# Kernel optimization log

Measured on AMD Instinct MI355X. Metric: run time of the kernel, lower is better.

The kernel has to match this reference:

```python
import jax, jax.numpy as jnp
import numpy as np

B = 2048        # batch
C = 64          # args.embed_size (channel dim; attention runs over this axis)
N = 11          # spatial rows per window
D = 11          # args.hsi_windowSize
SA = N * D      # args.size_SA = 121, Linear in/out size
HID = 128       # args.hid_router
NUM_PATH = 4    # num_out_path


def setup_inputs() -> dict:
    key = jax.random.key(0)
    ks = jax.random.split(key, 12)
    w = lambda k, shape: (jax.random.normal(k, shape, dtype=jnp.float32) * 0.05)
    return {
        "lidar": jax.random.normal(ks[0], (B, C, N, D), dtype=jnp.float32),
        "hsi": jax.random.normal(ks[1], (B, C, N, D), dtype=jnp.float32),
        # Cross_Self_attention linears (shared module, used in both directions)
        "Wq": w(ks[2], (SA, SA)), "bq": jnp.zeros((SA,), jnp.float32),
        "Wk": w(ks[3], (SA, SA)), "bk": jnp.zeros((SA,), jnp.float32),
        "Wv": w(ks[4], (SA, SA)), "bv": jnp.zeros((SA,), jnp.float32),
        # Router MLP: Linear(2C, HID) -> ReLU -> Linear(HID, NUM_PATH) -> softmax
        "Wr1": w(ks[5], (2 * C, HID)), "br1": jnp.zeros((HID,), jnp.float32),
        "Wr2": w(ks[6], (HID, NUM_PATH)), "br2": jnp.zeros((NUM_PATH,), jnp.float32),
        # 1x1 Conv2d(2C -> C): pure channel mixing
        "Wc": w(ks[7], (C, 2 * C)), "bc": jnp.zeros((C,), jnp.float32),
    }


def reference(lidar, hsi, Wq, bq, Wk, bk, Wv, bv, Wr1, br1, Wr2, br2, Wc, bc):
    def cross_sa(x, y):
        # x, y: [B, C, SA]; Linear acts on last dim (size_SA)
        q = x @ Wq.T + bq                                   # [B, C, SA]
        k = x @ Wk.T + bk                                   # [B, C, SA]
        v = y @ Wv.T + bv                                   # [B, C, SA]
        scores = jnp.einsum('bhs,bgs->bhg', q, k)           # [B, C, C] attn over channels
        probs = jax.nn.softmax(scores, axis=-1)
        # custom: attn @ (Q * V) elementwise gate instead of attn @ V
        return jnp.einsum('bhg,bgs->bhs', probs, q * v)     # [B, C, SA]
        # dropout(0.5) is identity in eval mode

    # router on channel-concat of raw inputs
    pooled = jnp.concatenate([lidar, hsi], axis=1).mean(axis=(2, 3))   # [B, 2C]
    path_prob = jax.nn.softmax(jax.nn.relu(pooled @ Wr1 + br1) @ Wr2 + br2, axis=-1)

    l = lidar.reshape(B, C, SA)
    h = hsi.reshape(B, C, SA)
    h_emb = cross_sa(l, h).reshape(B, C, N, D)
    l_emb = cross_sa(h, l).reshape(B, C, N, D)

    cat = jnp.concatenate([l_emb, h_emb], axis=1)                       # [B, 2C, N, D]
    emb = jnp.einsum('oc,bchw->bohw', Wc, cat) + bc[None, :, None, None]
    return (emb, path_prob)
```

## Files before the change

kernel.cpp:

```cpp
#include <hip/hip_runtime.h>
#include <hip/hip_bf16.h>

#define NB 2048
#define SA 121
#define EMB_TOTAL (NB * 64 * SA)

typedef short bf16x8 __attribute__((ext_vector_type(8)));
typedef float f32x4  __attribute__((ext_vector_type(4)));
typedef unsigned int u32x2 __attribute__((ext_vector_type(2)));

__device__ __forceinline__ short f2bf(float f) {
    union { __hip_bfloat16 h; short s; } u;
    u.h = __float2bfloat16(f);
    return u.s;
}
__device__ __forceinline__ float bf2f(short s) {
    union { unsigned u; float f; } v; v.u = ((unsigned)(unsigned short)s) << 16;
    return v.f;
}
__device__ __forceinline__ unsigned pack2(float a, float b) {
    union { __hip_bfloat16 h[2]; unsigned u; } p;
    p.h[0] = __float2bfloat16(a);
    p.h[1] = __float2bfloat16(b);
    return p.u;
}

#define MFMA(a, b, c) __builtin_amdgcn_mfma_f32_16x16x32_bf16((a), (b), (c), 0, 0, 0)

__global__ void convert_weights(const float* __restrict__ Wq, const float* __restrict__ Wk,
                                const float* __restrict__ Wv, const float* __restrict__ Wc,
                                short* __restrict__ ws) {
    int i = blockIdx.x * 256 + threadIdx.x;
    if (i < 49152) {
        int m = i / 16384;
        const float* W = (m == 0) ? Wq : ((m == 1) ? Wk : Wv);
        int j = i & 16383;
        int r = j >> 7, c = j & 127;
        float v = (r < SA && c < SA) ? W[r * SA + c] : 0.f;
        ws[i] = f2bf(v);
    } else {
        int j = i - 49152;
        ws[i] = f2bf(Wc[j]);
    }
}

__launch_bounds__(256, 2)
__global__ void fused_kernel(const float* __restrict__ lidar, const float* __restrict__ hsi,
                             const float* __restrict__ bq, const float* __restrict__ bk,
                             const float* __restrict__ bv,
                             const float* __restrict__ Wr1, const float* __restrict__ br1,
                             const float* __restrict__ Wr2, const float* __restrict__ br2,
                             const float* __restrict__ bc,
                             const short* __restrict__ wsb, float* __restrict__ out) {
    __shared__ __align__(16) short sA[64 * 136];
    __shared__ __align__(16) short sB[64 * 136];
    __shared__ __align__(16) short sC[64 * 136];
    __shared__ __align__(16) short sD[128 * 72];
    __shared__ __align__(16) short sE[64 * 72];
    __shared__ float sR[260];

    const int tid  = threadIdx.x;
    const int b    = blockIdx.x;
    const int lane = tid & 63;
    const int wid  = tid >> 6;
    const int l16  = lane & 15;
    const int g16  = lane >> 4;

    const short* WQ = wsb;
    const short* WK = wsb + 16384;
    const short* WV = wsb + 32768;
    const short* WC = wsb + 49152;

    bf16x8 wqf[2][4], wkf[2][4], wvf[2][4];
    #pragma unroll
    for (int nn = 0; nn < 2; ++nn) {
        const int rw = ((wid * 2 + nn) * 16 + l16) * 128 + g16 * 8;
        #pragma unroll
        for (int k0 = 0; k0 < 4; ++k0) {
            wqf[nn][k0] = *(const bf16x8*)&WQ[rw + k0 * 32];
            wkf[nn][k0] = *(const bf16x8*)&WK[rw + k0 * 32];
            wvf[nn][k0] = *(const bf16x8*)&WV[rw + k0 * 32];
        }
    }
    float bqv[2], bkv[2], bvv2[2];
    #pragma unroll
    for (int nn = 0; nn < 2; ++nn) {
        int sc_ = (wid * 2 + nn) * 16 + l16;
        bool ok = sc_ < SA;
        bqv[nn]  = ok ? bq[sc_] : 0.f;
        bkv[nn]  = ok ? bk[sc_] : 0.f;
        bvv2[nn] = ok ? bv[sc_] : 0.f;
    }

    {
        const int row = wid * 16 + l16;
        const float* gA = lidar + (size_t)b * 7744 + row * 121;
        const float* gB = hsi   + (size_t)b * 7744 + row * 121;
        float rsA = 0.f, rsB = 0.f;
        #pragma unroll
        for (int k0 = 0; k0 < 4; ++k0) {
            const int c0 = k0 * 32 + g16 * 8;
            bf16x8 a, h;
            if (c0 == 120) {
                float xa = gA[120], xb = gB[120];
                rsA += xa; rsB += xb;
                a[0] = f2bf(xa); h[0] = f2bf(xb);
                #pragma unroll
                for (int j = 1; j < 8; ++j) { a[j] = 0; h[j] = 0; }
            } else {
                #pragma unroll
                for (int j = 0; j < 8; ++j) {
                    float xa = gA[c0 + j], xb = gB[c0 + j];
                    rsA += xa; rsB += xb;
                    a[j] = f2bf(xa); h[j] = f2bf(xb);
                }
            }
            *(bf16x8*)&sA[row * 136 + c0] = a;
            *(bf16x8*)&sB[row * 136 + c0] = h;
        }
        rsA += __shfl_xor(rsA, 16, 64); rsA += __shfl_xor(rsA, 32, 64);
        rsB += __shfl_xor(rsB, 16, 64); rsB += __shfl_xor(rsB, 32, 64);
        if (g16 == 0) { sR[row] = rsA * (1.f / 121.f); sR[64 + row] = rsB * (1.f / 121.f); }
    }
    __syncthreads();

    f32x4 eacc[8];
    #pragma unroll
    for (int n = 0; n < 8; ++n) eacc[n] = (f32x4){0.f, 0.f, 0.f, 0.f};

    #pragma unroll 1
    for (int dir = 0; dir < 2; ++dir) {
        const short* Xqk = dir ? sB : sA;
        const short* Xv  = dir ? sA : sB;
        const int cb = dir ? 0 : 1;

        #pragma unroll
        for (int m = 0; m < 4; ++m) {
            bf16x8 afr[4];
            #pragma unroll
            for (int k0 = 0; k0 < 4; ++k0)
                afr[k0] = *(const bf16x8*)&Xqk[(m * 16 + l16) * 136 + k0 * 32 + g16 * 8];
            f32x4 qa[2], ka[2];
            qa[0] = (f32x4){0,0,0,0}; qa[1] = (f32x4){0,0,0,0};
            ka[0] = (f32x4){0,0,0,0}; ka[1] = (f32x4){0,0,0,0};
            #pragma unroll
            for (int k0 = 0; k0 < 4; ++k0)
                #pragma unroll
                for (int nn = 0; nn < 2; ++nn) {
                    qa[nn] = MFMA(afr[k0], wqf[nn][k0], qa[nn]);
                    ka[nn] = MFMA(afr[k0], wkf[nn][k0], ka[nn]);
                }
            #pragma unroll
            for (int nn = 0; nn < 2; ++nn) {
                int sc_ = (wid * 2 + nn) * 16 + l16;
                #pragma unroll
                for (int r = 0; r < 4; ++r) {
                    int row = m * 16 + g16 * 4 + r;
                    sC[row * 136 + sc_] = f2bf(qa[nn][r] + bqv[nn]);
                    sD[row * 136 + sc_] = f2bf(ka[nn][r] + bkv[nn]);
                }
            }
        }
        __syncthreads();

        {
            f32x4 sc4[4];
            #pragma unroll
            for (int n = 0; n < 4; ++n) sc4[n] = (f32x4){0,0,0,0};
            #pragma unroll
            for (int k0 = 0; k0 < 4; ++k0) {
                bf16x8 afr = *(const bf16x8*)&sC[(wid * 16 + l16) * 136 + k0 * 32 + g16 * 8];
                #pragma unroll
                for (int n = 0; n < 4; ++n) {
                    bf16x8 bfr = *(const bf16x8*)&sD[(n * 16 + l16) * 136 + k0 * 32 + g16 * 8];
                    sc4[n] = MFMA(afr, bfr, sc4[n]);
                }
            }
            float p[4][4];
            #pragma unroll
            for (int r = 0; r < 4; ++r) {
                float mx = fmaxf(fmaxf(sc4[0][r], sc4[1][r]), fmaxf(sc4[2][r], sc4[3][r]));
                #pragma unroll
                for (int off = 1; off < 16; off <<= 1) mx = fmaxf(mx, __shfl_xor(mx, off, 64));
                float e0 = exp2f((sc4[0][r] - mx) * 1.44269504f);
                float e1 = exp2f((sc4[1][r] - mx) * 1.44269504f);
                float e2 = exp2f((sc4[2][r] - mx) * 1.44269504f);
                float e3 = exp2f((sc4[3][r] - mx) * 1.44269504f);
                float sum = e0 + e1 + e2 + e3;
                #pragma unroll
                for (int off = 1; off < 16; off <<= 1) sum += __shfl_xor(sum, off, 64);
                float inv = 1.f / sum;
                p[0][r] = e0 * inv; p[1][r] = e1 * inv; p[2][r] = e2 * inv; p[3][r] = e3 * inv;
            }
            #pragma unroll
            for (int n = 0; n < 4; ++n) {
                u32x2 pk;
                pk.x = pack2(p[n][0], p[n][1]);
                pk.y = pack2(p[n][2], p[n][3]);
                *(u32x2*)&sE[(n * 16 + l16) * 72 + wid * 16 + g16 * 4] = pk;
            }
        }
        __syncthreads();

        {
            const int rwc = (wid * 16 + l16) * 128 + cb * 64 + g16 * 8;
            bf16x8 wc0 = *(const bf16x8*)&WC[rwc];
            bf16x8 wc1 = *(const bf16x8*)&WC[rwc + 32];
            f32x4 macc[4];
            #pragma unroll
            for (int n = 0; n < 4; ++n) macc[n] = (f32x4){0,0,0,0};
            #pragma unroll
            for (int n = 0; n < 4; ++n) {
                bf16x8 b0 = *(const bf16x8*)&sE[(n * 16 + l16) * 72 + g16 * 8];
                bf16x8 b1 = *(const bf16x8*)&sE[(n * 16 + l16) * 72 + 32 + g16 * 8];
                macc[n] = MFMA(wc0, b0, macc[n]);
                macc[n] = MFMA(wc1, b1, macc[n]);
            }
            #pragma unroll
            for (int m = 0; m < 4; ++m) {
                bf16x8 afr[4];
                #pragma unroll
                for (int k0 = 0; k0 < 4; ++k0)
                    afr[k0] = *(const bf16x8*)&Xv[(m * 16 + l16) * 136 + k0 * 32 + g16 * 8];
                f32x4 va[2];
                va[0] = (f32x4){0,0,0,0}; va[1] = (f32x4){0,0,0,0};
                #pragma unroll
                for (int k0 = 0; k0 < 4; ++k0)
                    #pragma unroll
                    for (int nn = 0; nn < 2; ++nn)
                        va[nn] = MFMA(afr[k0], wvf[nn][k0], va[nn]);
                #pragma unroll
                for (int nn = 0; nn < 2; ++nn) {
                    int sc_ = (wid * 2 + nn) * 16 + l16;
                    float q0 = bf2f(sC[(m * 16 + g16 * 4 + 0) * 136 + sc_]);
                    float q1 = bf2f(sC[(m * 16 + g16 * 4 + 1) * 136 + sc_]);
                    float q2 = bf2f(sC[(m * 16 + g16 * 4 + 2) * 136 + sc_]);
                    float q3 = bf2f(sC[(m * 16 + g16 * 4 + 3) * 136 + sc_]);
                    float g0 = (va[nn][0] + bvv2[nn]) * q0;
                    float g1 = (va[nn][1] + bvv2[nn]) * q1;
                    float g2 = (va[nn][2] + bvv2[nn]) * q2;
                    float g3 = (va[nn][3] + bvv2[nn]) * q3;
                    u32x2 pk;
                    pk.x = pack2(g0, g1);
                    pk.y = pack2(g2, g3);
                    *(u32x2*)&sD[sc_ * 72 + m * 16 + g16 * 4] = pk;
                }
            }
            __syncthreads();
            #pragma unroll
            for (int n = 0; n < 4; ++n)
                #pragma unroll
                for (int r = 0; r < 4; ++r) {
                    int o = wid * 16 + g16 * 4 + r;
                    sE[o * 72 + n * 16 + l16] = f2bf(macc[n][r]);
                }
        }

        #pragma unroll
        for (int k0 = 0; k0 < 2; ++k0) {
            bf16x8 afr = *(const bf16x8*)&sE[(wid * 16 + l16) * 72 + k0 * 32 + g16 * 8];
            #pragma unroll
            for (int n = 0; n < 8; ++n) {
                bf16x8 bfr = *(const bf16x8*)&sD[(n * 16 + l16) * 72 + k0 * 32 + g16 * 8];
                eacc[n] = MFMA(afr, bfr, eacc[n]);
            }
        }
        __syncthreads();
    }

    float* eo = out + (size_t)b * 7744;
    {
        float bcv[4];
        #pragma unroll
        for (int r = 0; r < 4; ++r) bcv[r] = bc[wid * 16 + g16 * 4 + r];
        #pragma unroll
        for (int n = 0; n < 8; ++n) {
            int s = n * 16 + l16;
            if (s < SA) {
                #pragma unroll
                for (int r = 0; r < 4; ++r) {
                    int o = wid * 16 + g16 * 4 + r;
                    eo[o * 121 + s] = eacc[n][r] + bcv[r];
                }
            }
        }
    }

    if (tid < 128) {
        float a[8];
        #pragma unroll
        for (int j = 0; j < 8; ++j) a[j] = 0.f;
        for (int c = 0; c < 128; c += 8) {
            #pragma unroll
            for (int j = 0; j < 8; ++j)
                a[j] += sR[c + j] * Wr1[(c + j) * 128 + tid];
        }
        float s01 = a[0] + a[1], s23 = a[2] + a[3], s45 = a[4] + a[5], s67 = a[6] + a[7];
        sR[128 + tid] = fmaxf((s01 + s23) + (s45 + s67) + br1[tid], 0.f);
    }
    __syncthreads();
    if (tid < 4) {
        float a[8];
        #pragma unroll
        for (int j = 0; j < 8; ++j) a[j] = 0.f;
        for (int h = 0; h < 128; h += 8) {
            #pragma unroll
            for (int j = 0; j < 8; ++j)
                a[j] += sR[128 + h + j] * Wr2[(h + j) * 4 + tid];
        }
        float s01 = a[0] + a[1], s23 = a[2] + a[3], s45 = a[4] + a[5], s67 = a[6] + a[7];
        sR[256 + tid] = (s01 + s23) + (s45 + s67) + br2[tid];
    }
    __syncthreads();
    if (tid < 4) {
        float m = fmaxf(fmaxf(sR[256], sR[257]), fmaxf(sR[258], sR[259]));
        float e = __expf(sR[256 + tid] - m);
        float s = 0.f;
        for (int p = 0; p < 4; ++p) s += __expf(sR[256 + p] - m);
        out[EMB_TOTAL + b * 4 + tid] = e / s;
    }
}

extern "C" void kernel_launch(void* const* d_in, const int* in_sizes, int n_in,
                              void* d_out, int out_size, void* d_ws, size_t ws_size,
                              hipStream_t stream) {
    const float* lidar = (const float*)d_in[0];
    const float* hsi   = (const float*)d_in[1];
    const float* Wq  = (const float*)d_in[2];  const float* bq  = (const float*)d_in[3];
    const float* Wk  = (const float*)d_in[4];  const float* bk  = (const float*)d_in[5];
    const float* Wv  = (const float*)d_in[6];  const float* bv  = (const float*)d_in[7];
    const float* Wr1 = (const float*)d_in[8];  const float* br1 = (const float*)d_in[9];
    const float* Wr2 = (const float*)d_in[10]; const float* br2 = (const float*)d_in[11];
    const float* Wc  = (const float*)d_in[12]; const float* bc  = (const float*)d_in[13];
    short* wsb = (short*)d_ws;
    float* out = (float*)d_out;

    hipLaunchKernelGGL(convert_weights, dim3(224), dim3(256), 0, stream, Wq, Wk, Wv, Wc, wsb);
    hipLaunchKernelGGL(fused_kernel, dim3(NB), dim3(256), 0, stream,
                       lidar, hsi, bq, bk, bv, Wr1, br1, Wr2, br2, bc, wsb, out);
}
```

Baseline: 109.2 us.

## Defer hsi staging past first attention phase and keep Q in registers

The hsi tile is loaded into registers at kernel start but converted and written to shared memory only after the dir-0 softmax, so its global latency overlaps the QK projection work. Q values are kept in fp32 registers for the gate product instead of being re-read from shared memory as bf16. Wv fragments are reloaded per direction rather than held across the whole kernel, and the final barrier is skipped on the last iteration. Together these aim to cut register pressure and load stalls, at the cost of 32 extra registers for the staged hsi values and repeated Wv loads. There is also a latent hazard: dir 0 reads Xv = sB in the QK loop before sB is written, but the V phase comes after the barrier, so this appears safe.

Measured after the change: 115.1 us. +5.4%, slower.

```diff
diff --git a/kernel.cpp b/kernel.cpp
--- a/kernel.cpp
+++ b/kernel.cpp
@@ -13,10 +13,6 @@
     union { __hip_bfloat16 h; short s; } u;
     u.h = __float2bfloat16(f);
     return u.s;
-}
-__device__ __forceinline__ float bf2f(short s) {
-    union { unsigned u; float f; } v; v.u = ((unsigned)(unsigned short)s) << 16;
-    return v.f;
 }
 __device__ __forceinline__ unsigned pack2(float a, float b) {
     union { __hip_bfloat16 h[2]; unsigned u; } p;
@@ -71,7 +67,7 @@
     const short* WV = wsb + 32768;
     const short* WC = wsb + 49152;
 
-    bf16x8 wqf[2][4], wkf[2][4], wvf[2][4];
+    bf16x8 wqf[2][4], wkf[2][4];
     #pragma unroll
     for (int nn = 0; nn < 2; ++nn) {
         const int rw = ((wid * 2 + nn) * 16 + l16) * 128 + g16 * 8;
@@ -79,7 +75,6 @@
         for (int k0 = 0; k0 < 4; ++k0) {
             wqf[nn][k0] = *(const bf16x8*)&WQ[rw + k0 * 32];
             wkf[nn][k0] = *(const bf16x8*)&WK[rw + k0 * 32];
-            wvf[nn][k0] = *(const bf16x8*)&WV[rw + k0 * 32];
         }
     }
     float bqv[2], bkv[2], bvv2[2];
@@ -92,35 +87,50 @@
         bvv2[nn] = ok ? bv[sc_] : 0.f;
     }
 
+    const int row = wid * 16 + l16;
+
+    float vb[32];
     {
-        const int row = wid * 16 + l16;
-        const float* gA = lidar + (size_t)b * 7744 + row * 121;
-        const float* gB = hsi   + (size_t)b * 7744 + row * 121;
-        float rsA = 0.f, rsB = 0.f;
+        const float* gB = hsi + (size_t)b * 7744 + row * 121;
         #pragma unroll
         for (int k0 = 0; k0 < 4; ++k0) {
             const int c0 = k0 * 32 + g16 * 8;
-            bf16x8 a, h;
             if (c0 == 120) {
-                float xa = gA[120], xb = gB[120];
-                rsA += xa; rsB += xb;
-                a[0] = f2bf(xa); h[0] = f2bf(xb);
-                #pragma unroll
-                for (int j = 1; j < 8; ++j) { a[j] = 0; h[j] = 0; }
+                vb[k0 * 8] = gB[120];
+                #pragma unroll
+                for (int j = 1; j < 8; ++j) vb[k0 * 8 + j] = 0.f;
             } else {
                 #pragma unroll
+                for (int j = 0; j < 8; ++j) vb[k0 * 8 + j] = gB[c0 + j];
+            }
+        }
+    }
+
+    {
+        const float* gA = lidar + (size_t)b * 7744 + row * 121;
+        float rsA = 0.f;
+        #pragma unroll
+        for (int k0 = 0; k0 < 4; ++k0) {
+            const int c0 = k0 * 32 + g16 * 8;
+            bf16x8 a;
+            if (c0 == 120) {
+                float xa = gA[120];
+                rsA += xa;
+                a[0] = f2bf(xa);
+                #pragma unroll
+                for (int j = 1; j < 8; ++j) a[j] = 0;
+            } else {
+                #pragma unroll
                 for (int j = 0; j < 8; ++j) {
-                    float xa = gA[c0 + j], xb = gB[c0 + j];
-                    rsA += xa; rsB += xb;
-                    a[j] = f2bf(xa); h[j] = f2bf(xb);
+                    float xa = gA[c0 + j];
+                    rsA += xa;
+                    a[j] = f2bf(xa);
                 }
             }
             *(bf16x8*)&sA[row * 136 + c0] = a;
-            *(bf16x8*)&sB[row * 136 + c0] = h;
         }
         rsA += __shfl_xor(rsA, 16, 64); rsA += __shfl_xor(rsA, 32, 64);
-        rsB += __shfl_xor(rsB, 16, 64); rsB += __shfl_xor(rsB, 32, 64);
-        if (g16 == 0) { sR[row] = rsA * (1.f / 121.f); sR[64 + row] = rsB * (1.f / 121.f); }
+        if (g16 == 0) sR[row] = rsA * (1.f / 121.f);
     }
     __syncthreads();
 
@@ -134,6 +144,8 @@
         const short* Xv  = dir ? sA : sB;
         const int cb = dir ? 0 : 1;
 
+        f32x4 qs[4][2];
+
         #pragma unroll
         for (int m = 0; m < 4; ++m) {
             bf16x8 afr[4];
@@ -155,9 +167,11 @@
                 int sc_ = (wid * 2 + nn) * 16 + l16;
                 #pragma unroll
                 for (int r = 0; r < 4; ++r) {
-                    int row = m * 16 + g16 * 4 + r;
-                    sC[row * 136 + sc_] = f2bf(qa[nn][r] + bqv[nn]);
-                    sD[row * 136 + sc_] = f2bf(ka[nn][r] + bkv[nn]);
+                    int row2 = m * 16 + g16 * 4 + r;
+                    float qv = qa[nn][r] + bqv[nn];
+                    qs[m][nn][r] = qv;
+                    sC[row2 * 136 + sc_] = f2bf(qv);
+                    sD[row2 * 136 + sc_] = f2bf(ka[nn][r] + bkv[nn]);
                 }
             }
         }
@@ -200,9 +214,34 @@
                 *(u32x2*)&sE[(n * 16 + l16) * 72 + wid * 16 + g16 * 4] = pk;
             }
         }
+
+        if (dir == 0) {
+            float rsB = 0.f;
+            #pragma unroll
+            for (int k0 = 0; k0 < 4; ++k0) {
+                const int c0 = k0 * 32 + g16 * 8;
+                bf16x8 h;
+                #pragma unroll
+                for (int j = 0; j < 8; ++j) {
+                    rsB += vb[k0 * 8 + j];
+                    h[j] = f2bf(vb[k0 * 8 + j]);
+                }
+                *(bf16x8*)&sB[row * 136 + c0] = h;
+            }
+            rsB += __shfl_xor(rsB, 16, 64); rsB += __shfl_xor(rsB, 32, 64);
+            if (g16 == 0) sR[64 + row] = rsB * (1.f / 121.f);
+        }
         __syncthreads();
 
         {
+            bf16x8 wvl[2][4];
+            #pragma unroll
+            for (int nn = 0; nn < 2; ++nn) {
+                const int rw = ((wid * 2 + nn) * 16 + l16) * 128 + g16 * 8;
+                #pragma unroll
+                for (int k0 = 0; k0 < 4; ++k0)
+                    wvl[nn][k0] = *(const bf16x8*)&WV[rw + k0 * 32];
+            }
             const int rwc = (wid * 16 + l16) * 128 + cb * 64 + g16 * 8;
             bf16x8 wc0 = *(const bf16x8*)&WC[rwc];
             bf16x8 wc1 = *(const bf16x8*)&WC[rwc + 32];
@@ -228,18 +267,14 @@
                 for (int k0 = 0; k0 < 4; ++k0)
                     #pragma unroll
                     for (int nn = 0; nn < 2; ++nn)
-                        va[nn] = MFMA(afr[k0], wvf[nn][k0], va[nn]);
+                        va[nn] = MFMA(afr[k0], wvl[nn][k0], va[nn]);
                 #pragma unroll
                 for (int nn = 0; nn < 2; ++nn) {
                     int sc_ = (wid * 2 + nn) * 16 + l16;
-                    float q0 = bf2f(sC[(m * 16 + g16 * 4 + 0) * 136 + sc_]);
-                    float q1 = bf2f(sC[(m * 16 + g16 * 4 + 1) * 136 + sc_]);
-                    float q2 = bf2f(sC[(m * 16 + g16 * 4 + 2) * 136 + sc_]);
-                    float q3 = bf2f(sC[(m * 16 + g16 * 4 + 3) * 136 + sc_]);
-                    float g0 = (va[nn][0] + bvv2[nn]) * q0;
-                    float g1 = (va[nn][1] + bvv2[nn]) * q1;
-                    float g2 = (va[nn][2] + bvv2[nn]) * q2;
-                    float g3 = (va[nn][3] + bvv2[nn]) * q3;
+                    float g0 = (va[nn][0] + bvv2[nn]) * qs[m][nn][0];
+                    float g1 = (va[nn][1] + bvv2[nn]) * qs[m][nn][1];
+                    float g2 = (va[nn][2] + bvv2[nn]) * qs[m][nn][2];
+                    float g3 = (va[nn][3] + bvv2[nn]) * qs[m][nn][3];
                     u32x2 pk;
                     pk.x = pack2(g0, g1);
                     pk.y = pack2(g2, g3);
@@ -265,7 +300,7 @@
                 eacc[n] = MFMA(afr, bfr, eacc[n]);
             }
         }
-        __syncthreads();
+        if (dir == 0) __syncthreads();
     }
 
     float* eo = out + (size_t)b * 7744;
```
